# Kernel tuning notes

Measured on AMD Instinct MI355X. Metric: run time of the kernel, lower is better.

Reference implementation:

```python
import jax, jax.numpy as jnp
import numpy as np


def setup_inputs() -> dict:
    key = jax.random.key(0)
    k1, k2 = jax.random.split(key)
    B, S, D = 64, 1024, 768
    batch = jax.random.normal(k1, (B, S, D), dtype=jnp.float32)
    # nn.init.uniform_(proj, -0.05, 0.05)
    proj = jax.random.uniform(k2, (D, D), minval=-0.05, maxval=0.05, dtype=jnp.float32)
    return {"batch": batch, "proj": proj}


def reference(batch, proj):
    """dists[b,i,j] = (h_i - h_j)^T A (h_i - h_j)
    Expanded: h_i^T A h_i + h_j^T A h_j - h_i^T A h_j - h_j^T A h_i.
    Avoids the O(B*S^2*D) diffs tensor of the original.
    """
    # P[b,i,:] = h_i^T A  -> (B, S, D)
    P = jnp.einsum('bid,de->bie', batch, proj)
    # cross[b,i,j] = h_i^T A h_j -> (B, S, S)
    cross = jnp.einsum('bie,bje->bij', P, batch)
    q = jnp.einsum('bii->bi', cross)  # h_i^T A h_i, (B, S)
    dists = q[:, :, None] + q[:, None, :] - cross - jnp.swapaxes(cross, 1, 2)
    return dists
```

## Files before the change

kernel.cpp:

```cpp
#include <hip/hip_runtime.h>

#define GLOBAL_AS __attribute__((address_space(1)))
#define LDS_AS    __attribute__((address_space(3)))

typedef __bf16 bf16_t;
typedef __bf16 bf16x8 __attribute__((ext_vector_type(8)));
typedef float  f32x4  __attribute__((ext_vector_type(4)));

#define BATCH 64
#define SEQ   1024
#define DIM   768
#define BS_ROWS (BATCH * SEQ)

__device__ __forceinline__ void gl2lds16(const void* g, void* l) {
    __builtin_amdgcn_global_load_lds((GLOBAL_AS const void*)g, (LDS_AS void*)l, 16, 0, 0);
}

__global__ void k_prep(const float* __restrict__ batch, const float* __restrict__ proj,
                       bf16_t* __restrict__ Hb, bf16_t* __restrict__ Ab) {
    int bid = blockIdx.x;
    if (bid < 24576) {
        int gid = bid * 256 + threadIdx.x;
        const float4* xp = (const float4*)batch;
        float4 a = xp[gid * 2];
        float4 b = xp[gid * 2 + 1];
        bf16x8 v;
        v[0] = (bf16_t)a.x; v[1] = (bf16_t)a.y; v[2] = (bf16_t)a.z; v[3] = (bf16_t)a.w;
        v[4] = (bf16_t)b.x; v[5] = (bf16_t)b.y; v[6] = (bf16_t)b.z; v[7] = (bf16_t)b.w;
        ((bf16x8*)Hb)[gid] = v;
    } else {
        int idx = (bid - 24576) * 256 + threadIdx.x;
        int d = idx / DIM;
        int e = idx - d * DIM;
        Ab[idx] = (bf16_t)(proj[idx] + proj[e * DIM + d]);
    }
}

__global__ void k_gemm1(const bf16_t* __restrict__ H, const bf16_t* __restrict__ Ag,
                        bf16_t* __restrict__ M) {
    __shared__ bf16_t Asm[128 * 32];
    __shared__ bf16_t Bsm[128 * 32];
    const int t = threadIdx.x;
    const int g = blockIdx.x;
    const int tile = (g & 7) * 384 + (g >> 3);
    const int row0 = (tile / 6) * 128;
    const int col0 = (tile % 6) * 128;
    const int ln = t & 63, w = t >> 6;
    const int wr = w >> 1, wc = w & 1;
    const int r = ln & 15, qd = ln >> 4;
    const int sseg = qd ^ ((r >> 1) & 3);

    const int srow = t >> 2;
    const int gseg = (t & 3) ^ ((t >> 3) & 3);
    const bf16_t* gA0 = H  + (size_t)(row0 + srow) * DIM + gseg * 8;
    const bf16_t* gA1 = gA0 + (size_t)64 * DIM;
    const bf16_t* gB0 = Ag + (size_t)(col0 + srow) * DIM + gseg * 8;
    const bf16_t* gB1 = gB0 + (size_t)64 * DIM;

    f32x4 acc[4][4] = {};

    for (int k0 = 0; k0 < DIM; k0 += 32) {
        gl2lds16(gA0 + k0, &Asm[t * 8]);
        gl2lds16(gA1 + k0, &Asm[2048 + t * 8]);
        gl2lds16(gB0 + k0, &Bsm[t * 8]);
        gl2lds16(gB1 + k0, &Bsm[2048 + t * 8]);
        __syncthreads();

        bf16x8 af[4], bf[4];
#pragma unroll
        for (int mt = 0; mt < 4; ++mt) {
            int m = wr * 64 + mt * 16 + r;
            af[mt] = *(const bf16x8*)&Asm[m * 32 + sseg * 8];
        }
#pragma unroll
        for (int nt = 0; nt < 4; ++nt) {
            int n = wc * 64 + nt * 16 + r;
            bf[nt] = *(const bf16x8*)&Bsm[n * 32 + sseg * 8];
        }
#pragma unroll
        for (int mt = 0; mt < 4; ++mt)
#pragma unroll
            for (int nt = 0; nt < 4; ++nt)
                acc[mt][nt] = __builtin_amdgcn_mfma_f32_16x16x32_bf16(
                    af[mt], bf[nt], acc[mt][nt], 0, 0, 0);
        __syncthreads();
    }

#pragma unroll
    for (int mt = 0; mt < 4; ++mt) {
#pragma unroll
        for (int rI = 0; rI < 4; ++rI) {
            int row = row0 + wr * 64 + mt * 16 + qd * 4 + rI;
            size_t base = (size_t)row * DIM + col0 + wc * 64;
#pragma unroll
            for (int nt = 0; nt < 4; ++nt)
                M[base + nt * 16 + r] = (bf16_t)acc[mt][nt][rI];
        }
    }
}

__global__ void k_g2diag(const bf16_t* __restrict__ M, const bf16_t* __restrict__ H,
                         float* __restrict__ qv, float* __restrict__ out) {
    __shared__ bf16_t Asm[128 * 32];
    __shared__ bf16_t Bsm[128 * 32];
    __shared__ float qsm[128];
    const int t = threadIdx.x;
    const int g = blockIdx.x;
    const int u = (g & 7) * 64 + (g >> 3);
    const int b = u >> 3;
    const int ti = u & 7;
    const int row0 = ti * 128;

    const int ln = t & 63, w = t >> 6;
    const int wr = w >> 1, wc = w & 1;
    const int r = ln & 15, qd = ln >> 4;
    const int sseg = qd ^ ((r >> 1) & 3);

    const bf16_t* Mb = M + (size_t)b * SEQ * DIM;
    const bf16_t* Hb = H + (size_t)b * SEQ * DIM;

    const int srow = t >> 2;
    const int gseg = (t & 3) ^ ((t >> 3) & 3);
    const bf16_t* gA0 = Mb + (size_t)(row0 + srow) * DIM + gseg * 8;
    const bf16_t* gA1 = gA0 + (size_t)64 * DIM;
    const bf16_t* gB0 = Hb + (size_t)(row0 + srow) * DIM + gseg * 8;
    const bf16_t* gB1 = gB0 + (size_t)64 * DIM;

    f32x4 acc[4][4] = {};
    float s0 = 0.f, s1 = 0.f;

    for (int k0 = 0; k0 < DIM; k0 += 32) {
        gl2lds16(gA0 + k0, &Asm[t * 8]);
        gl2lds16(gA1 + k0, &Asm[2048 + t * 8]);
        gl2lds16(gB0 + k0, &Bsm[t * 8]);
        gl2lds16(gB1 + k0, &Bsm[2048 + t * 8]);
        __syncthreads();

        bf16x8 va0 = *(const bf16x8*)&Asm[t * 8];
        bf16x8 vb0 = *(const bf16x8*)&Bsm[t * 8];
        bf16x8 va1 = *(const bf16x8*)&Asm[2048 + t * 8];
        bf16x8 vb1 = *(const bf16x8*)&Bsm[2048 + t * 8];
#pragma unroll
        for (int j = 0; j < 8; ++j) {
            s0 += (float)va0[j] * (float)vb0[j];
            s1 += (float)va1[j] * (float)vb1[j];
        }

        bf16x8 af[4], bfv[4];
#pragma unroll
        for (int mt = 0; mt < 4; ++mt) {
            int m = wr * 64 + mt * 16 + r;
            af[mt] = *(const bf16x8*)&Asm[m * 32 + sseg * 8];
        }
#pragma unroll
        for (int nt = 0; nt < 4; ++nt) {
            int n = wc * 64 + nt * 16 + r;
            bfv[nt] = *(const bf16x8*)&Bsm[n * 32 + sseg * 8];
        }
#pragma unroll
        for (int mt = 0; mt < 4; ++mt)
#pragma unroll
            for (int nt = 0; nt < 4; ++nt)
                acc[mt][nt] = __builtin_amdgcn_mfma_f32_16x16x32_bf16(
                    af[mt], bfv[nt], acc[mt][nt], 0, 0, 0);
        __syncthreads();
    }

    s0 += __shfl_xor(s0, 1, 64); s0 += __shfl_xor(s0, 2, 64);
    s1 += __shfl_xor(s1, 1, 64); s1 += __shfl_xor(s1, 2, 64);
    if ((t & 3) == 0) {
        float q0 = 0.5f * s0, q1 = 0.5f * s1;
        qsm[srow] = q0; qsm[64 + srow] = q1;
        qv[(size_t)b * SEQ + row0 + srow] = q0;
        qv[(size_t)b * SEQ + row0 + 64 + srow] = q1;
    }
    __syncthreads();

    float qc[4];
#pragma unroll
    for (int nt = 0; nt < 4; ++nt) qc[nt] = qsm[wc * 64 + nt * 16 + r];

#pragma unroll
    for (int mt = 0; mt < 4; ++mt) {
#pragma unroll
        for (int rI = 0; rI < 4; ++rI) {
            int lrow = wr * 64 + mt * 16 + qd * 4 + rI;
            float qr = qsm[lrow];
            size_t base = ((size_t)b * SEQ + row0 + lrow) * SEQ + row0 + wc * 64;
#pragma unroll
            for (int nt = 0; nt < 4; ++nt)
                out[base + nt * 16 + r] = qr + qc[nt] - acc[mt][nt][rI];
        }
    }
}

__global__ void k_g2off(const bf16_t* __restrict__ M, const bf16_t* __restrict__ H,
                        const float* __restrict__ qv, float* __restrict__ out) {
    __shared__ __align__(16) char smem[16640];
    bf16_t* Asm = (bf16_t*)smem;
    bf16_t* Bsm = (bf16_t*)(smem + 8192);
    float*  Tsm = (float*)smem;

    const int t = threadIdx.x;
    const int g = blockIdx.x;
    const int u = (g & 7) * 224 + (g >> 3);
    const int b = u / 28;
    int l = u - b * 28;
    int ti = 0;
    while (l >= 7 - ti) { l -= 7 - ti; ++ti; }
    const int tj = ti + 1 + l;
    const int row0 = ti * 128;
    const int col0 = tj * 128;

    const int ln = t & 63, w = t >> 6;
    const int wr = w >> 1, wc = w & 1;
    const int r = ln & 15, qd = ln >> 4;
    const int sseg = qd ^ ((r >> 1) & 3);

    const bf16_t* Mb = M + (size_t)b * SEQ * DIM;
    const bf16_t* Hb = H + (size_t)b * SEQ * DIM;

    const int srow = t >> 2;
    const int gseg = (t & 3) ^ ((t >> 3) & 3);
    const bf16_t* gA0 = Mb + (size_t)(row0 + srow) * DIM + gseg * 8;
    const bf16_t* gA1 = gA0 + (size_t)64 * DIM;
    const bf16_t* gB0 = Hb + (size_t)(col0 + srow) * DIM + gseg * 8;
    const bf16_t* gB1 = gB0 + (size_t)64 * DIM;

    f32x4 acc[4][4] = {};

    for (int k0 = 0; k0 < DIM; k0 += 32) {
        gl2lds16(gA0 + k0, &Asm[t * 8]);
        gl2lds16(gA1 + k0, &Asm[2048 + t * 8]);
        gl2lds16(gB0 + k0, &Bsm[t * 8]);
        gl2lds16(gB1 + k0, &Bsm[2048 + t * 8]);
        __syncthreads();

        bf16x8 af[4], bfv[4];
#pragma unroll
        for (int mt = 0; mt < 4; ++mt) {
            int m = wr * 64 + mt * 16 + r;
            af[mt] = *(const bf16x8*)&Asm[m * 32 + sseg * 8];
        }
#pragma unroll
        for (int nt = 0; nt < 4; ++nt) {
            int n = wc * 64 + nt * 16 + r;
            bfv[nt] = *(const bf16x8*)&Bsm[n * 32 + sseg * 8];
        }
#pragma unroll
        for (int mt = 0; mt < 4; ++mt)
#pragma unroll
            for (int nt = 0; nt < 4; ++nt)
                acc[mt][nt] = __builtin_amdgcn_mfma_f32_16x16x32_bf16(
                    af[mt], bfv[nt], acc[mt][nt], 0, 0, 0);
        __syncthreads();
    }

    const float* qb = qv + (size_t)b * SEQ;
    float qc[4];
#pragma unroll
    for (int nt = 0; nt < 4; ++nt) qc[nt] = qb[col0 + wc * 64 + nt * 16 + r];

#pragma unroll
    for (int mt = 0; mt < 4; ++mt) {
#pragma unroll
        for (int rI = 0; rI < 4; ++rI) {
            int row = row0 + wr * 64 + mt * 16 + qd * 4 + rI;
            float qr = qb[row];
            size_t base = ((size_t)b * SEQ + row) * SEQ + col0 + wc * 64;
#pragma unroll
            for (int nt = 0; nt < 4; ++nt)
                out[base + nt * 16 + r] = qr + qc[nt] - acc[mt][nt][rI];
        }
    }

#pragma unroll
    for (int c = 0; c < 4; ++c) {
        __syncthreads();
        if (wr == (c >> 1)) {
            const int m0 = (c & 1) * 2;
#pragma unroll
            for (int mi = 0; mi < 2; ++mi) {
                const int mt = m0 + mi;
#pragma unroll
                for (int rI = 0; rI < 4; ++rI) {
                    int lrow = mi * 16 + qd * 4 + rI;
                    int row = row0 + wr * 64 + mt * 16 + qd * 4 + rI;
                    float qr = qb[row];
#pragma unroll
                    for (int nt = 0; nt < 4; ++nt) {
                        int lcol = wc * 64 + nt * 16 + r;
                        Tsm[lrow * 130 + lcol] = qr + qc[nt] - acc[mt][nt][rI];
                    }
                }
            }
        }
        __syncthreads();
        const int rowbase = row0 + 32 * c;
#pragma unroll
        for (int i = 0; i < 16; ++i) {
            int lin = i * 256 + t;
            int lrow = lin & 31;
            int lcol = lin >> 5;
            out[((size_t)b * SEQ + col0 + lcol) * SEQ + rowbase + lrow] =
                Tsm[lrow * 130 + lcol];
        }
    }
}

extern "C" void kernel_launch(void* const* d_in, const int* in_sizes, int n_in,
                              void* d_out, int out_size, void* d_ws, size_t ws_size,
                              hipStream_t stream) {
    const float* batch = (const float*)d_in[0];
    const float* proj  = (const float*)d_in[1];
    float* out = (float*)d_out;

    char* ws = (char*)d_ws;
    bf16_t* Hb = (bf16_t*)ws;
    bf16_t* Mb = (bf16_t*)(ws + 100663296);
    bf16_t* Ab = (bf16_t*)(ws + 201326592);
    float*  qv = (float*)(ws + 202506240);

    k_prep<<<26880, 256, 0, stream>>>(batch, proj, Hb, Ab);
    k_gemm1<<<3072, 256, 0, stream>>>(Hb, Ab, Mb);
    k_g2diag<<<512, 256, 0, stream>>>(Mb, Hb, qv, out);
    k_g2off<<<1792, 256, 0, stream>>>(Mb, Hb, qv, out);
}
```

Measured before the change: 637.7 us.

## Double-buffer LDS with async prefetch two stages ahead in GEMM k-loops

Replaces the single-buffered 32-wide k-loop in the projection GEMM and the off-diagonal cross GEMM with a double-buffered 64-wide k-step pipeline. Global-to-LDS loads for stage kt+2 are issued while MFMAs for stage kt run, using explicit vmcnt/lgkmcnt waits and sched barriers in place of __syncthreads. This aims to hide global memory latency and halve the number of barrier round trips. LDS per block grows from about 16KB to 64KB, which may lower occupancy, and the hand-written waitcnt logic is fragile.

```diff
diff --git a/kernel.cpp b/kernel.cpp
--- a/kernel.cpp
+++ b/kernel.cpp
@@ -15,6 +15,8 @@
 __device__ __forceinline__ void gl2lds16(const void* g, void* l) {
     __builtin_amdgcn_global_load_lds((GLOBAL_AS const void*)g, (LDS_AS void*)l, 16, 0, 0);
 }
+
+#define SB() __builtin_amdgcn_sched_barrier(0)
 
 __global__ void k_prep(const float* __restrict__ batch, const float* __restrict__ proj,
                        bf16_t* __restrict__ Hb, bf16_t* __restrict__ Ab) {
@@ -36,10 +38,64 @@
     }
 }
 
+#define STAGE8(kt, buf) do {                                      \
+        int k0_ = (kt) * 64;                                      \
+        gl2lds16(gA0 + k0_,      &Adb[buf][t * 8]);               \
+        gl2lds16(gA1 + k0_,      &Adb[buf][2048 + t * 8]);        \
+        gl2lds16(gA0 + k0_ + 32, &Adb[buf][4096 + t * 8]);        \
+        gl2lds16(gA1 + k0_ + 32, &Adb[buf][6144 + t * 8]);        \
+        gl2lds16(gB0 + k0_,      &Bdb[buf][t * 8]);               \
+        gl2lds16(gB1 + k0_,      &Bdb[buf][2048 + t * 8]);        \
+        gl2lds16(gB0 + k0_ + 32, &Bdb[buf][4096 + t * 8]);        \
+        gl2lds16(gB1 + k0_ + 32, &Bdb[buf][6144 + t * 8]);        \
+    } while (0)
+
+#define KLOOP_PIPELINED()                                                     \
+    STAGE8(0, 0);                                                             \
+    STAGE8(1, 1);                                                             \
+    for (int kt = 0; kt < 12; ++kt) {                                         \
+        const int cur = kt & 1;                                               \
+        SB();                                                                 \
+        if (kt < 11) asm volatile("s_waitcnt vmcnt(8)" ::: "memory");         \
+        else         asm volatile("s_waitcnt vmcnt(0)" ::: "memory");         \
+        SB();                                                                 \
+        __builtin_amdgcn_s_barrier();      \
+        SB();                                                                 \
+        bf16x8 af[4][2], bfv[4][2];                                           \
+        _Pragma("unroll")                                                     \
+        for (int mt = 0; mt < 4; ++mt) {                                      \
+            int m = wr * 64 + mt * 16 + r;                                    \
+            _Pragma("unroll")                                                 \
+            for (int h = 0; h < 2; ++h)                                       \
+                af[mt][h] = *(const bf16x8*)&Adb[cur][h * 4096 + m * 32 + sseg * 8]; \
+        }                                                                     \
+        _Pragma("unroll")                                                     \
+        for (int nt = 0; nt < 4; ++nt) {                                      \
+            int n = wc * 64 + nt * 16 + r;                                    \
+            _Pragma("unroll")                                                 \
+            for (int h = 0; h < 2; ++h)                                       \
+                bfv[nt][h] = *(const bf16x8*)&Bdb[cur][h * 4096 + n * 32 + sseg * 8]; \
+        }                                                                     \
+        SB();                                                                 \
+        asm volatile("s_waitcnt lgkmcnt(0)" ::: "memory");                    \
+        SB();                                                                 \
+        __builtin_amdgcn_s_barrier();    \
+        SB();                                                                 \
+        if (kt < 10) STAGE8(kt + 2, cur);                                     \
+        _Pragma("unroll")                                                     \
+        for (int h = 0; h < 2; ++h)                                           \
+            _Pragma("unroll")                                                 \
+            for (int mt = 0; mt < 4; ++mt)                                    \
+                _Pragma("unroll")                                             \
+                for (int nt = 0; nt < 4; ++nt)                                \
+                    acc[mt][nt] = __builtin_amdgcn_mfma_f32_16x16x32_bf16(    \
+                        af[mt][h], bfv[nt][h], acc[mt][nt], 0, 0, 0);         \
+    }
+
 __global__ void k_gemm1(const bf16_t* __restrict__ H, const bf16_t* __restrict__ Ag,
                         bf16_t* __restrict__ M) {
-    __shared__ bf16_t Asm[128 * 32];
-    __shared__ bf16_t Bsm[128 * 32];
+    __shared__ bf16_t Adb[2][8192];
+    __shared__ bf16_t Bdb[2][8192];
     const int t = threadIdx.x;
     const int g = blockIdx.x;
     const int tile = (g & 7) * 384 + (g >> 3);
@@ -58,33 +114,7 @@
     const bf16_t* gB1 = gB0 + (size_t)64 * DIM;
 
     f32x4 acc[4][4] = {};
-
-    for (int k0 = 0; k0 < DIM; k0 += 32) {
-        gl2lds16(gA0 + k0, &Asm[t * 8]);
-        gl2lds16(gA1 + k0, &Asm[2048 + t * 8]);
-        gl2lds16(gB0 + k0, &Bsm[t * 8]);
-        gl2lds16(gB1 + k0, &Bsm[2048 + t * 8]);
-        __syncthreads();
-
-        bf16x8 af[4], bf[4];
-#pragma unroll
-        for (int mt = 0; mt < 4; ++mt) {
-            int m = wr * 64 + mt * 16 + r;
-            af[mt] = *(const bf16x8*)&Asm[m * 32 + sseg * 8];
-        }
-#pragma unroll
-        for (int nt = 0; nt < 4; ++nt) {
-            int n = wc * 64 + nt * 16 + r;
-            bf[nt] = *(const bf16x8*)&Bsm[n * 32 + sseg * 8];
-        }
-#pragma unroll
-        for (int mt = 0; mt < 4; ++mt)
-#pragma unroll
-            for (int nt = 0; nt < 4; ++nt)
-                acc[mt][nt] = __builtin_amdgcn_mfma_f32_16x16x32_bf16(
-                    af[mt], bf[nt], acc[mt][nt], 0, 0, 0);
-        __syncthreads();
-    }
+    KLOOP_PIPELINED();
 
 #pragma unroll
     for (int mt = 0; mt < 4; ++mt) {
@@ -196,10 +226,9 @@
 
 __global__ void k_g2off(const bf16_t* __restrict__ M, const bf16_t* __restrict__ H,
                         const float* __restrict__ qv, float* __restrict__ out) {
-    __shared__ __align__(16) char smem[16640];
-    bf16_t* Asm = (bf16_t*)smem;
-    bf16_t* Bsm = (bf16_t*)(smem + 8192);
-    float*  Tsm = (float*)smem;
+    __shared__ bf16_t Adb[2][8192];
+    __shared__ bf16_t Bdb[2][8192];
+    float* Tsm = (float*)&Adb[0][0];
 
     const int t = threadIdx.x;
     const int g = blockIdx.x;
@@ -228,33 +257,7 @@
     const bf16_t* gB1 = gB0 + (size_t)64 * DIM;
 
     f32x4 acc[4][4] = {};
-
-    for (int k0 = 0; k0 < DIM; k0 += 32) {
-        gl2lds16(gA0 + k0, &Asm[t * 8]);
-        gl2lds16(gA1 + k0, &Asm[2048 + t * 8]);
-        gl2lds16(gB0 + k0, &Bsm[t * 8]);
-        gl2lds16(gB1 + k0, &Bsm[2048 + t * 8]);
-        __syncthreads();
-
-        bf16x8 af[4], bfv[4];
-#pragma unroll
-        for (int mt = 0; mt < 4; ++mt) {
-            int m = wr * 64 + mt * 16 + r;
-            af[mt] = *(const bf16x8*)&Asm[m * 32 + sseg * 8];
-        }
-#pragma unroll
-        for (int nt = 0; nt < 4; ++nt) {
-            int n = wc * 64 + nt * 16 + r;
-            bfv[nt] = *(const bf16x8*)&Bsm[n * 32 + sseg * 8];
-        }
-#pragma unroll
-        for (int mt = 0; mt < 4; ++mt)
-#pragma unroll
-            for (int nt = 0; nt < 4; ++nt)
-                acc[mt][nt] = __builtin_amdgcn_mfma_f32_16x16x32_bf16(
-                    af[mt], bfv[nt], acc[mt][nt], 0, 0, 0);
-        __syncthreads();
-    }
+    KLOOP_PIPELINED();
 
     const float* qb = qv + (size_t)b * SEQ;
     float qc[4];
```

Measured after the change: 1.006 ms. +57.7%, slower.
